# Performance work log

Measured on AMD Instinct MI355X. Metric: run time of the kernel, lower is better.

The kernel has to match this reference:

```python
import jax, jax.numpy as jnp
import numpy as np

B, N, D, H = 2, 2048, 1024, 16
DH = D // H
SCALE = DH ** -0.5

def setup_inputs() -> dict:
    key = jax.random.key(0)
    k1, k2, k3 = jax.random.split(key, 3)
    x = jax.random.normal(k1, (B, N, D), dtype=jnp.float32)
    W_qkv = jax.random.normal(k2, (3 * D, D), dtype=jnp.float32) * (D ** -0.5)
    W_out = jax.random.normal(k3, (D, D), dtype=jnp.float32) * (D ** -0.5)
    mask = jnp.tril(jnp.ones((N, N), dtype=jnp.int32))  # causal mask; 0 -> -inf
    return {"x": x, "mask": mask, "W_qkv": W_qkv, "W_out": W_out}

def reference(x, mask, W_qkv, W_out):
    b, n, d = x.shape
    qkv = x @ W_qkv.T                                   # [B,N,3D]
    qkv = qkv.reshape(b, n, 3, H, DH).transpose(2, 0, 3, 1, 4)  # [3,B,H,N,DH]
    q, k, v = qkv[0], qkv[1], qkv[2]
    attn = jnp.einsum('bhqd,bhkd->bhqk', q, k) * SCALE  # [B,H,N,N]
    attn = jnp.where(mask == 0, -jnp.inf, attn)
    attn = jax.nn.softmax(attn, axis=-1)
    out = jnp.einsum('bhqk,bhkd->bhqd', attn, v)        # [B,H,N,DH]
    out = out.transpose(0, 2, 1, 3).reshape(b, n, d)    # [B,N,D]
    return out @ W_out.T
```

## Files before the change

### kernel.cpp

```cpp
#include <hip/hip_runtime.h>
#include <hip/hip_bf16.h>


typedef __hip_bfloat16 bf16;
typedef short bf16x8 __attribute__((ext_vector_type(8)));
typedef short bf16x4 __attribute__((ext_vector_type(4)));
typedef float f32x4 __attribute__((ext_vector_type(4)));

#define QSCALE 0.1803368801111204f

typedef __attribute__((address_space(3))) unsigned int lds_u32;
typedef const __attribute__((address_space(1))) unsigned int glob_u32;

__device__ __forceinline__ void glds16(const void* g, void* l) {
    __builtin_amdgcn_global_load_lds((glob_u32*)g, (lds_u32*)l, 16, 0, 0);
}

__device__ __forceinline__ short f2bf(float f) {
    __hip_bfloat16 h = __float2bfloat16(f);
    return *reinterpret_cast<short*>(&h);
}

__device__ __forceinline__ unsigned pack_bf16(float a, float b) {
    unsigned au = __builtin_bit_cast(unsigned, a) + 0x8000u;
    unsigned bu = __builtin_bit_cast(unsigned, b) + 0x8000u;
    return __builtin_amdgcn_perm(bu, au, 0x07060302u);
}

__global__ void cast_all(const float* __restrict__ x, const float* __restrict__ wqkv,
                         const float* __restrict__ wout, bf16* __restrict__ xb,
                         bf16* __restrict__ wqb, bf16* __restrict__ wob) {
    int i = blockIdx.x * blockDim.x + threadIdx.x;
    const float* src; bf16* dst; int off;
    if (i < 1048576)      { src = x;    dst = xb;  off = i; }
    else if (i < 1835008) { src = wqkv; dst = wqb; off = i - 1048576; }
    else                  { src = wout; dst = wob; off = i - 1835008; }
    float4 f = reinterpret_cast<const float4*>(src)[off];
    short4 s;
    s.x = f2bf(f.x); s.y = f2bf(f.y); s.z = f2bf(f.z); s.w = f2bf(f.w);
    reinterpret_cast<short4*>(dst)[off] = s;
}

template<int EPI>
__global__ __launch_bounds__(256)
void gemm128(const bf16* __restrict__ A, const bf16* __restrict__ Bt,
             float* __restrict__ Cf,
             bf16* __restrict__ qp, bf16* __restrict__ kp, bf16* __restrict__ vp,
             int K, int Ncols) {
    __shared__ alignas(16) short As[2][4096];
    __shared__ alignas(16) short Bs[2][4096];

    const int tid = threadIdx.x;
    const int wave = tid >> 6, lane = tid & 63;
    const int quad = lane >> 4, l16 = lane & 15;
    const int wm = wave >> 1, wn = wave & 1;
    const int m0 = blockIdx.x * 128;
    const int n0 = blockIdx.y * 128;

    f32x4 acc[4][4] = {};

    const int srow = tid >> 2;
    const int skk  = (((tid & 3) ^ ((tid >> 3) & 3))) * 8;
    const bf16* Ag = A  + (size_t)(m0 + srow) * K + skk;
    const bf16* Bg = Bt + (size_t)(n0 + srow) * K + skk;
    const size_t rowskip = (size_t)64 * K;
    short* Asl = &As[0][0] + tid * 8;
    short* Bsl = &Bs[0][0] + tid * 8;

    const int xk = (quad ^ ((l16 >> 1) & 3)) * 8;
    const int arow = wm * 64 + l16;
    const int brow = wn * 64 + l16;

    const int KI = K >> 5;
    glds16(Ag, Asl);
    glds16(Ag + rowskip, Asl + 2048);
    glds16(Bg, Bsl);
    glds16(Bg + rowskip, Bsl + 2048);
    __syncthreads();

    int buf = 0;
    for (int ki = 0; ki < KI; ++ki) {
        if (ki + 1 < KI) {
            const bf16* ag = Ag + (ki + 1) * 32;
            const bf16* bg = Bg + (ki + 1) * 32;
            short* ad = Asl + (buf ^ 1) * 4096;
            short* bd = Bsl + (buf ^ 1) * 4096;
            glds16(ag, ad);
            glds16(ag + rowskip, ad + 2048);
            glds16(bg, bd);
            glds16(bg + rowskip, bd + 2048);
        }
        const short* ab = &As[buf][0];
        const short* bb = &Bs[buf][0];
        bf16x8 af[4], bf[4];
        #pragma unroll
        for (int mt = 0; mt < 4; ++mt)
            af[mt] = *reinterpret_cast<const bf16x8*>(ab + (arow + mt * 16) * 32 + xk);
        #pragma unroll
        for (int nt = 0; nt < 4; ++nt)
            bf[nt] = *reinterpret_cast<const bf16x8*>(bb + (brow + nt * 16) * 32 + xk);
        #pragma unroll
        for (int mt = 0; mt < 4; ++mt)
            #pragma unroll
            for (int nt = 0; nt < 4; ++nt)
                acc[mt][nt] = __builtin_amdgcn_mfma_f32_16x16x32_bf16(
                    af[mt], bf[nt], acc[mt][nt], 0, 0, 0);
        __syncthreads();
        buf ^= 1;
    }

    #pragma unroll
    for (int mt = 0; mt < 4; ++mt) {
        #pragma unroll
        for (int nt = 0; nt < 4; ++nt) {
            #pragma unroll
            for (int r = 0; r < 4; ++r) {
                int gm = m0 + wm * 64 + mt * 16 + quad * 4 + r;
                int gn = n0 + wn * 64 + nt * 16 + l16;
                float val = acc[mt][nt][r];
                if (EPI == 0) {
                    int sel = gn >> 10, rem = gn & 1023;
                    int h = rem >> 6, dh = rem & 63;
                    int b = gm >> 11, nq = gm & 2047;
                    if (sel == 0) val *= QSCALE;
                    bf16* dst = (sel == 0) ? qp : ((sel == 1) ? kp : vp);
                    dst[((((size_t)b * 16 + h) * 2048) + nq) * 64 + dh] = __float2bfloat16(val);
                } else {
                    Cf[(size_t)gm * Ncols + gn] = val;
                }
            }
        }
    }
}

__device__ __forceinline__ void attn_segment(
    const bf16* __restrict__ Qb, const bf16* __restrict__ Kb,
    const bf16* __restrict__ Vb, bf16* __restrict__ ao,
    float* __restrict__ Pslot, float* __restrict__ Lslot,
    short (*Ks)[64][72], short (*Vt)[64][68],
    int Q0, int jt0, int ntiles, bool withDiag, bool finalOut,
    int wave, int quad, int l16, int tid, int b, int h)
{
    const float NEG_INF = -__builtin_inff();
    const int qrowA = Q0 + wave * 16 + l16;
    const int qrowB = qrowA + 64;
    const bf16x8 qfA0 = *reinterpret_cast<const bf16x8*>(Qb + (size_t)qrowA * 64 + quad * 8);
    const bf16x8 qfA1 = *reinterpret_cast<const bf16x8*>(Qb + (size_t)qrowA * 64 + 32 + quad * 8);
    const bf16x8 qfB0 = *reinterpret_cast<const bf16x8*>(Qb + (size_t)qrowB * 64 + quad * 8);
    const bf16x8 qfB1 = *reinterpret_cast<const bf16x8*>(Qb + (size_t)qrowB * 64 + 32 + quad * 8);

    float lA = 0.f, lB = 0.f;
    f32x4 oA[4] = {}, oB[4] = {};

    const int krow = tid >> 2, kcol = (tid & 3) * 16;
    const int kb = (tid & 15) * 4, db = (tid >> 4) * 4;

    __syncthreads();
    {
        const bf16* K0 = Kb + (size_t)jt0 * 4096;
        const bf16* V0 = Vb + (size_t)jt0 * 4096;
        bf16x8 a0 = *reinterpret_cast<const bf16x8*>(K0 + (size_t)krow * 64 + kcol);
        bf16x8 a1 = *reinterpret_cast<const bf16x8*>(K0 + (size_t)krow * 64 + kcol + 8);
        bf16x4 L0 = *reinterpret_cast<const bf16x4*>(V0 + (size_t)(kb + 0) * 64 + db);
        bf16x4 L1 = *reinterpret_cast<const bf16x4*>(V0 + (size_t)(kb + 1) * 64 + db);
        bf16x4 L2 = *reinterpret_cast<const bf16x4*>(V0 + (size_t)(kb + 2) * 64 + db);
        bf16x4 L3 = *reinterpret_cast<const bf16x4*>(V0 + (size_t)(kb + 3) * 64 + db);
        *reinterpret_cast<bf16x8*>(&Ks[0][krow][kcol]) = a0;
        *reinterpret_cast<bf16x8*>(&Ks[0][krow][kcol + 8]) = a1;
        #pragma unroll
        for (int j = 0; j < 4; ++j) {
            bf16x4 w; w[0] = L0[j]; w[1] = L1[j]; w[2] = L2[j]; w[3] = L3[j];
            *reinterpret_cast<bf16x4*>(&Vt[0][db + j][kb]) = w;
        }
    }
    __syncthreads();

    int buf = 0;
    for (int i = 0; i < ntiles; ++i) {
        const bool diagA = withDiag && (i == ntiles - 2);
        const bool diagB = withDiag && (i == ntiles - 1);
        const bool pre = (i + 1 < ntiles);

        bf16x8 nk0, nk1; bf16x4 N0, N1, N2, N3;
        if (pre) {
            const bf16* Kn = Kb + (size_t)(jt0 + i + 1) * 4096;
            const bf16* Vn = Vb + (size_t)(jt0 + i + 1) * 4096;
            nk0 = *reinterpret_cast<const bf16x8*>(Kn + (size_t)krow * 64 + kcol);
            nk1 = *reinterpret_cast<const bf16x8*>(Kn + (size_t)krow * 64 + kcol + 8);
            N0 = *reinterpret_cast<const bf16x4*>(Vn + (size_t)(kb + 0) * 64 + db);
            N1 = *reinterpret_cast<const bf16x4*>(Vn + (size_t)(kb + 1) * 64 + db);
            N2 = *reinterpret_cast<const bf16x4*>(Vn + (size_t)(kb + 2) * 64 + db);
            N3 = *reinterpret_cast<const bf16x4*>(Vn + (size_t)(kb + 3) * 64 + db);
        }

        bf16x4 pkA[4], pkB[4];
        if (!diagA && !diagB) {
            #pragma unroll
            for (int t = 0; t < 4; ++t) {
                bf16x8 k0 = *reinterpret_cast<const bf16x8*>(&Ks[buf][16 * t + l16][quad * 8]);
                bf16x8 k1 = *reinterpret_cast<const bf16x8*>(&Ks[buf][16 * t + l16][32 + quad * 8]);
                f32x4 sA = {}, sB = {};
                sA = __builtin_amdgcn_mfma_f32_16x16x32_bf16(k0, qfA0, sA, 0, 0, 0);
                sA = __builtin_amdgcn_mfma_f32_16x16x32_bf16(k1, qfA1, sA, 0, 0, 0);
                sB = __builtin_amdgcn_mfma_f32_16x16x32_bf16(k0, qfB0, sB, 0, 0, 0);
                sB = __builtin_amdgcn_mfma_f32_16x16x32_bf16(k1, qfB1, sB, 0, 0, 0);
                float a0 = __builtin_amdgcn_exp2f(sA[0]);
                float a1 = __builtin_amdgcn_exp2f(sA[1]);
                float a2 = __builtin_amdgcn_exp2f(sA[2]);
                float a3 = __builtin_amdgcn_exp2f(sA[3]);
                float b0 = __builtin_amdgcn_exp2f(sB[0]);
                float b1 = __builtin_amdgcn_exp2f(sB[1]);
                float b2 = __builtin_amdgcn_exp2f(sB[2]);
                float b3 = __builtin_amdgcn_exp2f(sB[3]);
                lA += (a0 + a1) + (a2 + a3);
                lB += (b0 + b1) + (b2 + b3);
                unsigned* pa = reinterpret_cast<unsigned*>(&pkA[t]);
                pa[0] = pack_bf16(a0, a1); pa[1] = pack_bf16(a2, a3);
                unsigned* pb = reinterpret_cast<unsigned*>(&pkB[t]);
                pb[0] = pack_bf16(b0, b1); pb[1] = pack_bf16(b2, b3);
            }
            #pragma unroll
            for (int t = 0; t < 4; ++t)
                #pragma unroll
                for (int dt = 0; dt < 4; ++dt) {
                    bf16x4 vf = *reinterpret_cast<const bf16x4*>(
                        &Vt[buf][dt * 16 + l16][t * 16 + quad * 4]);
                    oA[dt] = __builtin_amdgcn_mfma_f32_16x16x16bf16_1k(vf, pkA[t], oA[dt], 0, 0, 0);
                    oB[dt] = __builtin_amdgcn_mfma_f32_16x16x16bf16_1k(vf, pkB[t], oB[dt], 0, 0, 0);
                }
        } else if (diagA) {
            #pragma unroll
            for (int t = 0; t < 4; ++t) {
                bf16x8 k0 = *reinterpret_cast<const bf16x8*>(&Ks[buf][16 * t + l16][quad * 8]);
                bf16x8 k1 = *reinterpret_cast<const bf16x8*>(&Ks[buf][16 * t + l16][32 + quad * 8]);
                f32x4 sB = {};
                sB = __builtin_amdgcn_mfma_f32_16x16x32_bf16(k0, qfB0, sB, 0, 0, 0);
                sB = __builtin_amdgcn_mfma_f32_16x16x32_bf16(k1, qfB1, sB, 0, 0, 0);
                float b0 = __builtin_amdgcn_exp2f(sB[0]);
                float b1 = __builtin_amdgcn_exp2f(sB[1]);
                float b2 = __builtin_amdgcn_exp2f(sB[2]);
                float b3 = __builtin_amdgcn_exp2f(sB[3]);
                lB += (b0 + b1) + (b2 + b3);
                unsigned* pb = reinterpret_cast<unsigned*>(&pkB[t]);
                pb[0] = pack_bf16(b0, b1); pb[1] = pack_bf16(b2, b3);
                if (t <= wave) {
                    f32x4 sA = {};
                    sA = __builtin_amdgcn_mfma_f32_16x16x32_bf16(k0, qfA0, sA, 0, 0, 0);
                    sA = __builtin_amdgcn_mfma_f32_16x16x32_bf16(k1, qfA1, sA, 0, 0, 0);
                    if (t == wave) {
                        #pragma unroll
                        for (int r = 0; r < 4; ++r)
                            if (quad * 4 + r > l16) sA[r] = NEG_INF;
                    }
                    float a0 = __builtin_amdgcn_exp2f(sA[0]);
                    float a1 = __builtin_amdgcn_exp2f(sA[1]);
                    float a2 = __builtin_amdgcn_exp2f(sA[2]);
                    float a3 = __builtin_amdgcn_exp2f(sA[3]);
                    lA += (a0 + a1) + (a2 + a3);
                    unsigned* pa = reinterpret_cast<unsigned*>(&pkA[t]);
                    pa[0] = pack_bf16(a0, a1); pa[1] = pack_bf16(a2, a3);
                }
            }
            #pragma unroll
            for (int t = 0; t < 4; ++t)
                #pragma unroll
                for (int dt = 0; dt < 4; ++dt) {
                    bf16x4 vf = *reinterpret_cast<const bf16x4*>(
                        &Vt[buf][dt * 16 + l16][t * 16 + quad * 4]);
                    oB[dt] = __builtin_amdgcn_mfma_f32_16x16x16bf16_1k(vf, pkB[t], oB[dt], 0, 0, 0);
                    if (t <= wave)
                        oA[dt] = __builtin_amdgcn_mfma_f32_16x16x16bf16_1k(vf, pkA[t], oA[dt], 0, 0, 0);
                }
        } else {
            #pragma unroll
            for (int t = 0; t < 4; ++t) {
                if (t <= wave) {
                    bf16x8 k0 = *reinterpret_cast<const bf16x8*>(&Ks[buf][16 * t + l16][quad * 8]);
                    bf16x8 k1 = *reinterpret_cast<const bf16x8*>(&Ks[buf][16 * t + l16][32 + quad * 8]);
                    f32x4 sB = {};
                    sB = __builtin_amdgcn_mfma_f32_16x16x32_bf16(k0, qfB0, sB, 0, 0, 0);
                    sB = __builtin_amdgcn_mfma_f32_16x16x32_bf16(k1, qfB1, sB, 0, 0, 0);
                    if (t == wave) {
                        #pragma unroll
                        for (int r = 0; r < 4; ++r)
                            if (quad * 4 + r > l16) sB[r] = NEG_INF;
                    }
                    float b0 = __builtin_amdgcn_exp2f(sB[0]);
                    float b1 = __builtin_amdgcn_exp2f(sB[1]);
                    float b2 = __builtin_amdgcn_exp2f(sB[2]);
                    float b3 = __builtin_amdgcn_exp2f(sB[3]);
                    lB += (b0 + b1) + (b2 + b3);
                    unsigned* pb = reinterpret_cast<unsigned*>(&pkB[t]);
                    pb[0] = pack_bf16(b0, b1); pb[1] = pack_bf16(b2, b3);
                }
            }
            #pragma unroll
            for (int t = 0; t < 4; ++t) {
                if (t <= wave) {
                    #pragma unroll
                    for (int dt = 0; dt < 4; ++dt) {
                        bf16x4 vf = *reinterpret_cast<const bf16x4*>(
                            &Vt[buf][dt * 16 + l16][t * 16 + quad * 4]);
                        oB[dt] = __builtin_amdgcn_mfma_f32_16x16x16bf16_1k(vf, pkB[t], oB[dt], 0, 0, 0);
                    }
                }
            }
        }

        if (pre) {
            *reinterpret_cast<bf16x8*>(&Ks[buf ^ 1][krow][kcol]) = nk0;
            *reinterpret_cast<bf16x8*>(&Ks[buf ^ 1][krow][kcol + 8]) = nk1;
            #pragma unroll
            for (int j = 0; j < 4; ++j) {
                bf16x4 w; w[0] = N0[j]; w[1] = N1[j]; w[2] = N2[j]; w[3] = N3[j];
                *reinterpret_cast<bf16x4*>(&Vt[buf ^ 1][db + j][kb]) = w;
            }
            __syncthreads();
            buf ^= 1;
        }
    }

    if (finalOut) {
        lA += __shfl_xor(lA, 16, 64);
        lA += __shfl_xor(lA, 32, 64);
        lB += __shfl_xor(lB, 16, 64);
        lB += __shfl_xor(lB, 32, 64);
        const float invA = 1.f / lA;
        const float invB = 1.f / lB;
        bf16* orowA = ao + ((size_t)b * 2048 + qrowA) * 1024 + h * 64;
        bf16* orowB = ao + ((size_t)b * 2048 + qrowB) * 1024 + h * 64;
        #pragma unroll
        for (int dt = 0; dt < 4; ++dt) {
            bf16x4 wA, wB;
            unsigned* ua = reinterpret_cast<unsigned*>(&wA);
            ua[0] = pack_bf16(oA[dt][0] * invA, oA[dt][1] * invA);
            ua[1] = pack_bf16(oA[dt][2] * invA, oA[dt][3] * invA);
            *reinterpret_cast<bf16x4*>(orowA + dt * 16 + quad * 4) = wA;
            unsigned* ub = reinterpret_cast<unsigned*>(&wB);
            ub[0] = pack_bf16(oB[dt][0] * invB, oB[dt][1] * invB);
            ub[1] = pack_bf16(oB[dt][2] * invB, oB[dt][3] * invB);
            *reinterpret_cast<bf16x4*>(orowB + dt * 16 + quad * 4) = wB;
        }
    } else {
        const int rrA = wave * 16 + l16;
        float* pA = Pslot + rrA * 64;
        float* pB = Pslot + (rrA + 64) * 64;
        #pragma unroll
        for (int dt = 0; dt < 4; ++dt) {
            *reinterpret_cast<f32x4*>(pA + dt * 16 + quad * 4) = oA[dt];
            *reinterpret_cast<f32x4*>(pB + dt * 16 + quad * 4) = oB[dt];
        }
        lA += __shfl_xor(lA, 16, 64);
        lA += __shfl_xor(lA, 32, 64);
        lB += __shfl_xor(lB, 16, 64);
        lB += __shfl_xor(lB, 32, 64);
        if (quad == 0) {
            Lslot[rrA] = lA;
            Lslot[rrA + 64] = lB;
        }
    }
}

__global__ __launch_bounds__(256)
void flash_split(const bf16* __restrict__ Q, const bf16* __restrict__ K,
                 const bf16* __restrict__ V, float* __restrict__ Ppart,
                 float* __restrict__ Lpart, bf16* __restrict__ ao) {
    __shared__ alignas(16) short Ks[2][64][72];
    __shared__ alignas(16) short Vt[2][64][68];

    const int tid = threadIdx.x;
    const int wave = tid >> 6, lane = tid & 63;
    const int quad = lane >> 4, l16 = lane & 15;
    const int bh = blockIdx.x;
    const int ys = blockIdx.y;
    const int p = ys & 7;
    const int qhi = 15 - p;
    const int b = bh >> 4, h = bh & 15;

    const bf16* Qb = Q + (size_t)bh * 2048 * 64;
    const bf16* Kb = K + (size_t)bh * 2048 * 64;
    const bf16* Vb = V + (size_t)bh * 2048 * 64;

    if (ys < 8) {
        attn_segment(Qb, Kb, Vb, ao, nullptr, nullptr, Ks, Vt,
                     p * 128, 0, 2 * p + 2, true, true,
                     wave, quad, l16, tid, b, h);
        float* Ps = Ppart + (size_t)(bh * 8 + p) * 8192;
        float* Ls = Lpart + (size_t)(bh * 8 + p) * 128;
        attn_segment(Qb, Kb, Vb, ao, Ps, Ls, Ks, Vt,
                     qhi * 128, 0, 15 - 2 * p, false, false,
                     wave, quad, l16, tid, b, h);
    } else {
        float* Ps = Ppart + (size_t)(256 + bh * 8 + p) * 8192;
        float* Ls = Lpart + (size_t)(256 + bh * 8 + p) * 128;
        attn_segment(Qb, Kb, Vb, ao, Ps, Ls, Ks, Vt,
                     qhi * 128, 15 - 2 * p, 17, true, false,
                     wave, quad, l16, tid, b, h);
    }
}

__global__ __launch_bounds__(256)
void combine(const float* __restrict__ Ppart, const float* __restrict__ Lpart,
             bf16* __restrict__ ao) {
    const int s = blockIdx.x;
    const int bh = s >> 3, p = s & 7;
    const int Q0 = (15 - p) * 128;
    const int b = bh >> 4, h = bh & 15;
    const int rr = threadIdx.x >> 1;
    const int dh0 = (threadIdx.x & 1) * 32;

    const float* p0 = Ppart + (size_t)s * 8192 + rr * 64 + dh0;
    const float* p1 = Ppart + (size_t)(256 + s) * 8192 + rr * 64 + dh0;
    const float inv = 1.f / (Lpart[(size_t)s * 128 + rr] +
                             Lpart[(size_t)(256 + s) * 128 + rr]);
    bf16* dst = ao + ((size_t)b * 2048 + Q0 + rr) * 1024 + h * 64 + dh0;
    #pragma unroll
    for (int j = 0; j < 32; j += 8) {
        f32x4 a0 = *reinterpret_cast<const f32x4*>(p0 + j);
        f32x4 a1 = *reinterpret_cast<const f32x4*>(p0 + j + 4);
        f32x4 c0 = *reinterpret_cast<const f32x4*>(p1 + j);
        f32x4 c1 = *reinterpret_cast<const f32x4*>(p1 + j + 4);
        bf16x8 w;
        unsigned* u = reinterpret_cast<unsigned*>(&w);
        u[0] = pack_bf16((a0[0] + c0[0]) * inv, (a0[1] + c0[1]) * inv);
        u[1] = pack_bf16((a0[2] + c0[2]) * inv, (a0[3] + c0[3]) * inv);
        u[2] = pack_bf16((a1[0] + c1[0]) * inv, (a1[1] + c1[1]) * inv);
        u[3] = pack_bf16((a1[2] + c1[2]) * inv, (a1[3] + c1[3]) * inv);
        *reinterpret_cast<bf16x8*>(dst + j) = w;
    }
}

extern "C" void kernel_launch(void* const* d_in, const int* in_sizes, int n_in,
                              void* d_out, int out_size, void* d_ws, size_t ws_size,
                              hipStream_t stream) {
    const float* x    = (const float*)d_in[0];
    const float* Wqkv = (const float*)d_in[2];
    const float* Wout = (const float*)d_in[3];
    float* out = (float*)d_out;

    char* ws = (char*)d_ws;
    bf16*  x_bf    = (bf16*)(ws);
    bf16*  wqkv_bf = (bf16*)(ws + (8ull << 20));
    float* Ppart   = (float*)(ws);
    bf16*  q       = (bf16*)(ws + (16ull << 20));
    bf16*  k       = (bf16*)(ws + (24ull << 20));
    bf16*  v       = (bf16*)(ws + (32ull << 20));
    bf16*  ao      = (bf16*)(ws + (40ull << 20));
    bf16*  wout_bf = (bf16*)(ws + (48ull << 20));
    float* Lpart   = (float*)(ws + (50ull << 20));

    cast_all<<<8192, 256, 0, stream>>>(x, Wqkv, Wout, x_bf, wqkv_bf, wout_bf);
    gemm128<0><<<dim3(32, 24), 256, 0, stream>>>(x_bf, wqkv_bf, nullptr, q, k, v, 1024, 3072);
    flash_split<<<dim3(32, 16), 256, 0, stream>>>(q, k, v, Ppart, Lpart, ao);
    combine<<<256, 256, 0, stream>>>(Ppart, Lpart, ao);
    gemm128<1><<<dim3(32, 8), 256, 0, stream>>>(ao, wout_bf, out, nullptr, nullptr, nullptr, 1024, 1024);
}
```

Measured before the change: 186.5 us.

## Split causal attention work into four balanced KV chunks per pair

The flash kernel now launches twice as many blocks. Each paired query tile's 34 KV tiles are split into four roughly equal chunks, and partial outputs are stored in bf16 instead of fp32. The combine kernel sums up to four partials per tile and also handles the low tiles that were split. This aims to improve load balance and occupancy (launch bounds 256,4) and to cut partial-output traffic, at the cost of more combine work and bf16 rounding in the unnormalised partial sums.

```diff
diff --git a/kernel.cpp b/kernel.cpp
--- a/kernel.cpp
+++ b/kernel.cpp
@@ -133,158 +133,140 @@
     }
 }
 
-__device__ __forceinline__ void attn_segment(
-    const bf16* __restrict__ Qb, const bf16* __restrict__ Kb,
-    const bf16* __restrict__ Vb, bf16* __restrict__ ao,
-    float* __restrict__ Pslot, float* __restrict__ Lslot,
-    short (*Ks)[64][72], short (*Vt)[64][68],
-    int Q0, int jt0, int ntiles, bool withDiag, bool finalOut,
-    int wave, int quad, int l16, int tid, int b, int h)
-{
+__global__ __launch_bounds__(256, 4)
+void flash_split(const bf16* __restrict__ Q, const bf16* __restrict__ K,
+                 const bf16* __restrict__ V, bf16* __restrict__ Opart,
+                 float* __restrict__ Lpart, bf16* __restrict__ ao) {
+    __shared__ alignas(16) short Ks[2][64][72];
+    __shared__ alignas(16) short Vt[2][64][68];
+
+    const int tid = threadIdx.x;
+    const int wave = tid >> 6, lane = tid & 63;
+    const int quad = lane >> 4, l16 = lane & 15;
+    const int bh = blockIdx.x;
+    const int y = blockIdx.y;
+    const int p = y >> 2, c = y & 3;
+    const int TL = 2 * p + 2;
+    const int a  = (c == 0) ? 0 : (c == 1) ? 9 : (c == 2) ? 18 : 26;
+    const int bnd = a + ((c < 2) ? 9 : 8);
+    const int b = bh >> 4, h = bh & 15;
     const float NEG_INF = -__builtin_inff();
-    const int qrowA = Q0 + wave * 16 + l16;
-    const int qrowB = qrowA + 64;
-    const bf16x8 qfA0 = *reinterpret_cast<const bf16x8*>(Qb + (size_t)qrowA * 64 + quad * 8);
-    const bf16x8 qfA1 = *reinterpret_cast<const bf16x8*>(Qb + (size_t)qrowA * 64 + 32 + quad * 8);
-    const bf16x8 qfB0 = *reinterpret_cast<const bf16x8*>(Qb + (size_t)qrowB * 64 + quad * 8);
-    const bf16x8 qfB1 = *reinterpret_cast<const bf16x8*>(Qb + (size_t)qrowB * 64 + 32 + quad * 8);
-
-    float lA = 0.f, lB = 0.f;
-    f32x4 oA[4] = {}, oB[4] = {};
+
+    const bf16* Qb = Q + (size_t)bh * 2048 * 64;
+    const bf16* Kb = K + (size_t)bh * 2048 * 64;
+    const bf16* Vb = V + (size_t)bh * 2048 * 64;
+
+    const int le0 = (bnd < TL) ? bnd : TL;
+    const bool hasLo = (a < le0);
+    const int hs = ((a > TL) ? a : TL) - TL;
+    const int he = bnd - TL;
+    const bool hasHi = (he > hs);
+    const int nseg = (hasLo ? 1 : 0) + (hasHi ? 1 : 0);
 
     const int krow = tid >> 2, kcol = (tid & 3) * 16;
     const int kb = (tid & 15) * 4, db = (tid >> 4) * 4;
 
-    __syncthreads();
-    {
-        const bf16* K0 = Kb + (size_t)jt0 * 4096;
-        const bf16* V0 = Vb + (size_t)jt0 * 4096;
-        bf16x8 a0 = *reinterpret_cast<const bf16x8*>(K0 + (size_t)krow * 64 + kcol);
-        bf16x8 a1 = *reinterpret_cast<const bf16x8*>(K0 + (size_t)krow * 64 + kcol + 8);
-        bf16x4 L0 = *reinterpret_cast<const bf16x4*>(V0 + (size_t)(kb + 0) * 64 + db);
-        bf16x4 L1 = *reinterpret_cast<const bf16x4*>(V0 + (size_t)(kb + 1) * 64 + db);
-        bf16x4 L2 = *reinterpret_cast<const bf16x4*>(V0 + (size_t)(kb + 2) * 64 + db);
-        bf16x4 L3 = *reinterpret_cast<const bf16x4*>(V0 + (size_t)(kb + 3) * 64 + db);
-        *reinterpret_cast<bf16x8*>(&Ks[0][krow][kcol]) = a0;
-        *reinterpret_cast<bf16x8*>(&Ks[0][krow][kcol + 8]) = a1;
-        #pragma unroll
-        for (int j = 0; j < 4; ++j) {
-            bf16x4 w; w[0] = L0[j]; w[1] = L1[j]; w[2] = L2[j]; w[3] = L3[j];
-            *reinterpret_cast<bf16x4*>(&Vt[0][db + j][kb]) = w;
-        }
-    }
-    __syncthreads();
-
-    int buf = 0;
-    for (int i = 0; i < ntiles; ++i) {
-        const bool diagA = withDiag && (i == ntiles - 2);
-        const bool diagB = withDiag && (i == ntiles - 1);
-        const bool pre = (i + 1 < ntiles);
-
-        bf16x8 nk0, nk1; bf16x4 N0, N1, N2, N3;
-        if (pre) {
-            const bf16* Kn = Kb + (size_t)(jt0 + i + 1) * 4096;
-            const bf16* Vn = Vb + (size_t)(jt0 + i + 1) * 4096;
-            nk0 = *reinterpret_cast<const bf16x8*>(Kn + (size_t)krow * 64 + kcol);
-            nk1 = *reinterpret_cast<const bf16x8*>(Kn + (size_t)krow * 64 + kcol + 8);
-            N0 = *reinterpret_cast<const bf16x4*>(Vn + (size_t)(kb + 0) * 64 + db);
-            N1 = *reinterpret_cast<const bf16x4*>(Vn + (size_t)(kb + 1) * 64 + db);
-            N2 = *reinterpret_cast<const bf16x4*>(Vn + (size_t)(kb + 2) * 64 + db);
-            N3 = *reinterpret_cast<const bf16x4*>(Vn + (size_t)(kb + 3) * 64 + db);
-        }
-
-        bf16x4 pkA[4], pkB[4];
-        if (!diagA && !diagB) {
-            #pragma unroll
-            for (int t = 0; t < 4; ++t) {
-                bf16x8 k0 = *reinterpret_cast<const bf16x8*>(&Ks[buf][16 * t + l16][quad * 8]);
-                bf16x8 k1 = *reinterpret_cast<const bf16x8*>(&Ks[buf][16 * t + l16][32 + quad * 8]);
-                f32x4 sA = {}, sB = {};
-                sA = __builtin_amdgcn_mfma_f32_16x16x32_bf16(k0, qfA0, sA, 0, 0, 0);
-                sA = __builtin_amdgcn_mfma_f32_16x16x32_bf16(k1, qfA1, sA, 0, 0, 0);
-                sB = __builtin_amdgcn_mfma_f32_16x16x32_bf16(k0, qfB0, sB, 0, 0, 0);
-                sB = __builtin_amdgcn_mfma_f32_16x16x32_bf16(k1, qfB1, sB, 0, 0, 0);
-                float a0 = __builtin_amdgcn_exp2f(sA[0]);
-                float a1 = __builtin_amdgcn_exp2f(sA[1]);
-                float a2 = __builtin_amdgcn_exp2f(sA[2]);
-                float a3 = __builtin_amdgcn_exp2f(sA[3]);
-                float b0 = __builtin_amdgcn_exp2f(sB[0]);
-                float b1 = __builtin_amdgcn_exp2f(sB[1]);
-                float b2 = __builtin_amdgcn_exp2f(sB[2]);
-                float b3 = __builtin_amdgcn_exp2f(sB[3]);
-                lA += (a0 + a1) + (a2 + a3);
-                lB += (b0 + b1) + (b2 + b3);
-                unsigned* pa = reinterpret_cast<unsigned*>(&pkA[t]);
-                pa[0] = pack_bf16(a0, a1); pa[1] = pack_bf16(a2, a3);
-                unsigned* pb = reinterpret_cast<unsigned*>(&pkB[t]);
-                pb[0] = pack_bf16(b0, b1); pb[1] = pack_bf16(b2, b3);
-            }
-            #pragma unroll
-            for (int t = 0; t < 4; ++t)
-                #pragma unroll
-                for (int dt = 0; dt < 4; ++dt) {
-                    bf16x4 vf = *reinterpret_cast<const bf16x4*>(
-                        &Vt[buf][dt * 16 + l16][t * 16 + quad * 4]);
-                    oA[dt] = __builtin_amdgcn_mfma_f32_16x16x16bf16_1k(vf, pkA[t], oA[dt], 0, 0, 0);
-                    oB[dt] = __builtin_amdgcn_mfma_f32_16x16x16bf16_1k(vf, pkB[t], oB[dt], 0, 0, 0);
-                }
-        } else if (diagA) {
-            #pragma unroll
-            for (int t = 0; t < 4; ++t) {
-                bf16x8 k0 = *reinterpret_cast<const bf16x8*>(&Ks[buf][16 * t + l16][quad * 8]);
-                bf16x8 k1 = *reinterpret_cast<const bf16x8*>(&Ks[buf][16 * t + l16][32 + quad * 8]);
-                f32x4 sB = {};
-                sB = __builtin_amdgcn_mfma_f32_16x16x32_bf16(k0, qfB0, sB, 0, 0, 0);
-                sB = __builtin_amdgcn_mfma_f32_16x16x32_bf16(k1, qfB1, sB, 0, 0, 0);
-                float b0 = __builtin_amdgcn_exp2f(sB[0]);
-                float b1 = __builtin_amdgcn_exp2f(sB[1]);
-                float b2 = __builtin_amdgcn_exp2f(sB[2]);
-                float b3 = __builtin_amdgcn_exp2f(sB[3]);
-                lB += (b0 + b1) + (b2 + b3);
-                unsigned* pb = reinterpret_cast<unsigned*>(&pkB[t]);
-                pb[0] = pack_bf16(b0, b1); pb[1] = pack_bf16(b2, b3);
-                if (t <= wave) {
-                    f32x4 sA = {};
+    for (int sgi = 0; sgi < nseg; ++sgi) {
+        const bool isLo = hasLo && (sgi == 0);
+        const int Q0  = (isLo ? p : (15 - p)) * 128;
+        const int jt0 = isLo ? a : hs;
+        const int nt  = isLo ? (le0 - a) : (he - hs);
+        const int T   = isLo ? TL : (34 - TL);
+        const bool fin = isLo && (a == 0) && (le0 == TL);
+        const int slot = ((bh * 8 + p) * 2 + (isLo ? 0 : 1)) * 4 + c;
+
+        const int qrowA = Q0 + wave * 16 + l16;
+        const int qrowB = qrowA + 64;
+        const bf16x8 qfA0 = *reinterpret_cast<const bf16x8*>(Qb + (size_t)qrowA * 64 + quad * 8);
+        const bf16x8 qfA1 = *reinterpret_cast<const bf16x8*>(Qb + (size_t)qrowA * 64 + 32 + quad * 8);
+        const bf16x8 qfB0 = *reinterpret_cast<const bf16x8*>(Qb + (size_t)qrowB * 64 + quad * 8);
+        const bf16x8 qfB1 = *reinterpret_cast<const bf16x8*>(Qb + (size_t)qrowB * 64 + 32 + quad * 8);
+
+        float lA = 0.f, lB = 0.f;
+        f32x4 oA[4] = {}, oB[4] = {};
+
+        __syncthreads();
+        {
+            const bf16* K0 = Kb + (size_t)jt0 * 4096;
+            const bf16* V0 = Vb + (size_t)jt0 * 4096;
+            bf16x8 a0 = *reinterpret_cast<const bf16x8*>(K0 + (size_t)krow * 64 + kcol);
+            bf16x8 a1 = *reinterpret_cast<const bf16x8*>(K0 + (size_t)krow * 64 + kcol + 8);
+            bf16x4 L0 = *reinterpret_cast<const bf16x4*>(V0 + (size_t)(kb + 0) * 64 + db);
+            bf16x4 L1 = *reinterpret_cast<const bf16x4*>(V0 + (size_t)(kb + 1) * 64 + db);
+            bf16x4 L2 = *reinterpret_cast<const bf16x4*>(V0 + (size_t)(kb + 2) * 64 + db);
+            bf16x4 L3 = *reinterpret_cast<const bf16x4*>(V0 + (size_t)(kb + 3) * 64 + db);
+            *reinterpret_cast<bf16x8*>(&Ks[0][krow][kcol]) = a0;
+            *reinterpret_cast<bf16x8*>(&Ks[0][krow][kcol + 8]) = a1;
+            #pragma unroll
+            for (int j = 0; j < 4; ++j) {
+                bf16x4 w; w[0] = L0[j]; w[1] = L1[j]; w[2] = L2[j]; w[3] = L3[j];
+                *reinterpret_cast<bf16x4*>(&Vt[0][db + j][kb]) = w;
+            }
+        }
+        __syncthreads();
+
+        int buf = 0;
+        for (int i = 0; i < nt; ++i) {
+            const int jabs = jt0 + i;
+            const bool diagA = (jabs == T - 2);
+            const bool diagB = (jabs == T - 1);
+            const bool pre = (i + 1 < nt);
+
+            bf16x8 nk0, nk1; bf16x4 N0, N1, N2, N3;
+            if (pre) {
+                const bf16* Kn = Kb + (size_t)(jabs + 1) * 4096;
+                const bf16* Vn = Vb + (size_t)(jabs + 1) * 4096;
+                nk0 = *reinterpret_cast<const bf16x8*>(Kn + (size_t)krow * 64 + kcol);
+                nk1 = *reinterpret_cast<const bf16x8*>(Kn + (size_t)krow * 64 + kcol + 8);
+                N0 = *reinterpret_cast<const bf16x4*>(Vn + (size_t)(kb + 0) * 64 + db);
+                N1 = *reinterpret_cast<const bf16x4*>(Vn + (size_t)(kb + 1) * 64 + db);
+                N2 = *reinterpret_cast<const bf16x4*>(Vn + (size_t)(kb + 2) * 64 + db);
+                N3 = *reinterpret_cast<const bf16x4*>(Vn + (size_t)(kb + 3) * 64 + db);
+            }
+
+            bf16x4 pkA[4], pkB[4];
+            if (!diagA && !diagB) {
+                #pragma unroll
+                for (int t = 0; t < 4; ++t) {
+                    bf16x8 k0 = *reinterpret_cast<const bf16x8*>(&Ks[buf][16 * t + l16][quad * 8]);
+                    bf16x8 k1 = *reinterpret_cast<const bf16x8*>(&Ks[buf][16 * t + l16][32 + quad * 8]);
+                    f32x4 sA = {}, sB = {};
                     sA = __builtin_amdgcn_mfma_f32_16x16x32_bf16(k0, qfA0, sA, 0, 0, 0);
                     sA = __builtin_amdgcn_mfma_f32_16x16x32_bf16(k1, qfA1, sA, 0, 0, 0);
-                    if (t == wave) {
-                        #pragma unroll
-                        for (int r = 0; r < 4; ++r)
-                            if (quad * 4 + r > l16) sA[r] = NEG_INF;
-                    }
+                    sB = __builtin_amdgcn_mfma_f32_16x16x32_bf16(k0, qfB0, sB, 0, 0, 0);
+                    sB = __builtin_amdgcn_mfma_f32_16x16x32_bf16(k1, qfB1, sB, 0, 0, 0);
                     float a0 = __builtin_amdgcn_exp2f(sA[0]);
                     float a1 = __builtin_amdgcn_exp2f(sA[1]);
                     float a2 = __builtin_amdgcn_exp2f(sA[2]);
                     float a3 = __builtin_amdgcn_exp2f(sA[3]);
+                    float b0 = __builtin_amdgcn_exp2f(sB[0]);
+                    float b1 = __builtin_amdgcn_exp2f(sB[1]);
+                    float b2 = __builtin_amdgcn_exp2f(sB[2]);
+                    float b3 = __builtin_amdgcn_exp2f(sB[3]);
                     lA += (a0 + a1) + (a2 + a3);
+                    lB += (b0 + b1) + (b2 + b3);
                     unsigned* pa = reinterpret_cast<unsigned*>(&pkA[t]);
                     pa[0] = pack_bf16(a0, a1); pa[1] = pack_bf16(a2, a3);
-                }
-            }
-            #pragma unroll
-            for (int t = 0; t < 4; ++t)
-                #pragma unroll
-                for (int dt = 0; dt < 4; ++dt) {
-                    bf16x4 vf = *reinterpret_cast<const bf16x4*>(
-                        &Vt[buf][dt * 16 + l16][t * 16 + quad * 4]);
-                    oB[dt] = __builtin_amdgcn_mfma_f32_16x16x16bf16_1k(vf, pkB[t], oB[dt], 0, 0, 0);
-                    if (t <= wave)
+                    unsigned* pb = reinterpret_cast<unsigned*>(&pkB[t]);
+                    pb[0] = pack_bf16(b0, b1); pb[1] = pack_bf16(b2, b3);
+                }
+                #pragma unroll
+                for (int t = 0; t < 4; ++t)
+                    #pragma unroll
+                    for (int dt = 0; dt < 4; ++dt) {
+                        bf16x4 vf = *reinterpret_cast<const bf16x4*>(
+                            &Vt[buf][dt * 16 + l16][t * 16 + quad * 4]);
                         oA[dt] = __builtin_amdgcn_mfma_f32_16x16x16bf16_1k(vf, pkA[t], oA[dt], 0, 0, 0);
-                }
-        } else {
-            #pragma unroll
-            for (int t = 0; t < 4; ++t) {
-                if (t <= wave) {
+                        oB[dt] = __builtin_amdgcn_mfma_f32_16x16x16bf16_1k(vf, pkB[t], oB[dt], 0, 0, 0);
+                    }
+            } else if (diagA) {
+                #pragma unroll
+                for (int t = 0; t < 4; ++t) {
                     bf16x8 k0 = *reinterpret_cast<const bf16x8*>(&Ks[buf][16 * t + l16][quad * 8]);
                     bf16x8 k1 = *reinterpret_cast<const bf16x8*>(&Ks[buf][16 * t + l16][32 + quad * 8]);
                     f32x4 sB = {};
                     sB = __builtin_amdgcn_mfma_f32_16x16x32_bf16(k0, qfB0, sB, 0, 0, 0);
                     sB = __builtin_amdgcn_mfma_f32_16x16x32_bf16(k1, qfB1, sB, 0, 0, 0);
-                    if (t == wave) {
-                        #pragma unroll
-                        for (int r = 0; r < 4; ++r)
-                            if (quad * 4 + r > l16) sB[r] = NEG_INF;
-                    }
                     float b0 = __builtin_amdgcn_exp2f(sB[0]);
                     float b1 = __builtin_amdgcn_exp2f(sB[1]);
                     float b2 = __builtin_amdgcn_exp2f(sB[2]);
@@ -292,141 +274,165 @@
                     lB += (b0 + b1) + (b2 + b3);
                     unsigned* pb = reinterpret_cast<unsigned*>(&pkB[t]);
                     pb[0] = pack_bf16(b0, b1); pb[1] = pack_bf16(b2, b3);
-                }
-            }
-            #pragma unroll
-            for (int t = 0; t < 4; ++t) {
-                if (t <= wave) {
+                    if (t <= wave) {
+                        f32x4 sA = {};
+                        sA = __builtin_amdgcn_mfma_f32_16x16x32_bf16(k0, qfA0, sA, 0, 0, 0);
+                        sA = __builtin_amdgcn_mfma_f32_16x16x32_bf16(k1, qfA1, sA, 0, 0, 0);
+                        if (t == wave) {
+                            #pragma unroll
+                            for (int r = 0; r < 4; ++r)
+                                if (quad * 4 + r > l16) sA[r] = NEG_INF;
+                        }
+                        float a0 = __builtin_amdgcn_exp2f(sA[0]);
+                        float a1 = __builtin_amdgcn_exp2f(sA[1]);
+                        float a2 = __builtin_amdgcn_exp2f(sA[2]);
+                        float a3 = __builtin_amdgcn_exp2f(sA[3]);
+                        lA += (a0 + a1) + (a2 + a3);
+                        unsigned* pa = reinterpret_cast<unsigned*>(&pkA[t]);
+                        pa[0] = pack_bf16(a0, a1); pa[1] = pack_bf16(a2, a3);
+                    }
+                }
+                #pragma unroll
+                for (int t = 0; t < 4; ++t)
                     #pragma unroll
                     for (int dt = 0; dt < 4; ++dt) {
                         bf16x4 vf = *reinterpret_cast<const bf16x4*>(
                             &Vt[buf][dt * 16 + l16][t * 16 + quad * 4]);
                         oB[dt] = __builtin_amdgcn_mfma_f32_16x16x16bf16_1k(vf, pkB[t], oB[dt], 0, 0, 0);
+                        if (t <= wave)
+                            oA[dt] = __builtin_amdgcn_mfma_f32_16x16x16bf16_1k(vf, pkA[t], oA[dt], 0, 0, 0);
                     }
-                }
-            }
-        }
-
-        if (pre) {
-            *reinterpret_cast<bf16x8*>(&Ks[buf ^ 1][krow][kcol]) = nk0;
-            *reinterpret_cast<bf16x8*>(&Ks[buf ^ 1][krow][kcol + 8]) = nk1;
-            #pragma unroll
-            for (int j = 0; j < 4; ++j) {
-                bf16x4 w; w[0] = N0[j]; w[1] = N1[j]; w[2] = N2[j]; w[3] = N3[j];
-                *reinterpret_cast<bf16x4*>(&Vt[buf ^ 1][db + j][kb]) = w;
-            }
-            __syncthreads();
-            buf ^= 1;
-        }
-    }
-
-    if (finalOut) {
+            } else {
+                #pragma unroll
+                for (int t = 0; t < 4; ++t) {
+                    if (t <= wave) {
+                        bf16x8 k0 = *reinterpret_cast<const bf16x8*>(&Ks[buf][16 * t + l16][quad * 8]);
+                        bf16x8 k1 = *reinterpret_cast<const bf16x8*>(&Ks[buf][16 * t + l16][32 + quad * 8]);
+                        f32x4 sB = {};
+                        sB = __builtin_amdgcn_mfma_f32_16x16x32_bf16(k0, qfB0, sB, 0, 0, 0);
+                        sB = __builtin_amdgcn_mfma_f32_16x16x32_bf16(k1, qfB1, sB, 0, 0, 0);
+                        if (t == wave) {
+                            #pragma unroll
+                            for (int r = 0; r < 4; ++r)
+                                if (quad * 4 + r > l16) sB[r] = NEG_INF;
+                        }
+                        float b0 = __builtin_amdgcn_exp2f(sB[0]);
+                        float b1 = __builtin_amdgcn_exp2f(sB[1]);
+                        float b2 = __builtin_amdgcn_exp2f(sB[2]);
+                        float b3 = __builtin_amdgcn_exp2f(sB[3]);
+                        lB += (b0 + b1) + (b2 + b3);
+                        unsigned* pb = reinterpret_cast<unsigned*>(&pkB[t]);
+                        pb[0] = pack_bf16(b0, b1); pb[1] = pack_bf16(b2, b3);
+                    }
+                }
+                #pragma unroll
+                for (int t = 0; t < 4; ++t) {
+                    if (t <= wave) {
+                        #pragma unroll
+                        for (int dt = 0; dt < 4; ++dt) {
+                            bf16x4 vf = *reinterpret_cast<const bf16x4*>(
+                                &Vt[buf][dt * 16 + l16][t * 16 + quad * 4]);
+                            oB[dt] = __builtin_amdgcn_mfma_f32_16x16x16bf16_1k(vf, pkB[t], oB[dt], 0, 0, 0);
+                        }
+                    }
+                }
+            }
+
+            if (pre) {
+                *reinterpret_cast<bf16x8*>(&Ks[buf ^ 1][krow][kcol]) = nk0;
+                *reinterpret_cast<bf16x8*>(&Ks[buf ^ 1][krow][kcol + 8]) = nk1;
+                #pragma unroll
+                for (int j = 0; j < 4; ++j) {
+                    bf16x4 w; w[0] = N0[j]; w[1] = N1[j]; w[2] = N2[j]; w[3] = N3[j];
+                    *reinterpret_cast<bf16x4*>(&Vt[buf ^ 1][db + j][kb]) = w;
+                }
+                __syncthreads();
+                buf ^= 1;
+            }
+        }
+
         lA += __shfl_xor(lA, 16, 64);
         lA += __shfl_xor(lA, 32, 64);
         lB += __shfl_xor(lB, 16, 64);
         lB += __shfl_xor(lB, 32, 64);
-        const float invA = 1.f / lA;
-        const float invB = 1.f / lB;
-        bf16* orowA = ao + ((size_t)b * 2048 + qrowA) * 1024 + h * 64;
-        bf16* orowB = ao + ((size_t)b * 2048 + qrowB) * 1024 + h * 64;
-        #pragma unroll
-        for (int dt = 0; dt < 4; ++dt) {
-            bf16x4 wA, wB;
-            unsigned* ua = reinterpret_cast<unsigned*>(&wA);
-            ua[0] = pack_bf16(oA[dt][0] * invA, oA[dt][1] * invA);
-            ua[1] = pack_bf16(oA[dt][2] * invA, oA[dt][3] * invA);
-            *reinterpret_cast<bf16x4*>(orowA + dt * 16 + quad * 4) = wA;
-            unsigned* ub = reinterpret_cast<unsigned*>(&wB);
-            ub[0] = pack_bf16(oB[dt][0] * invB, oB[dt][1] * invB);
-            ub[1] = pack_bf16(oB[dt][2] * invB, oB[dt][3] * invB);
-            *reinterpret_cast<bf16x4*>(orowB + dt * 16 + quad * 4) = wB;
-        }
-    } else {
-        const int rrA = wave * 16 + l16;
-        float* pA = Pslot + rrA * 64;
-        float* pB = Pslot + (rrA + 64) * 64;
-        #pragma unroll
-        for (int dt = 0; dt < 4; ++dt) {
-            *reinterpret_cast<f32x4*>(pA + dt * 16 + quad * 4) = oA[dt];
-            *reinterpret_cast<f32x4*>(pB + dt * 16 + quad * 4) = oB[dt];
-        }
-        lA += __shfl_xor(lA, 16, 64);
-        lA += __shfl_xor(lA, 32, 64);
-        lB += __shfl_xor(lB, 16, 64);
-        lB += __shfl_xor(lB, 32, 64);
-        if (quad == 0) {
-            Lslot[rrA] = lA;
-            Lslot[rrA + 64] = lB;
+        const int rr = wave * 16 + l16;
+        if (fin) {
+            const float invA = 1.f / lA;
+            const float invB = 1.f / lB;
+            bf16* orowA = ao + ((size_t)b * 2048 + qrowA) * 1024 + h * 64;
+            bf16* orowB = ao + ((size_t)b * 2048 + qrowB) * 1024 + h * 64;
+            #pragma unroll
+            for (int dt = 0; dt < 4; ++dt) {
+                bf16x4 wA, wB;
+                unsigned* ua = reinterpret_cast<unsigned*>(&wA);
+                ua[0] = pack_bf16(oA[dt][0] * invA, oA[dt][1] * invA);
+                ua[1] = pack_bf16(oA[dt][2] * invA, oA[dt][3] * invA);
+                *reinterpret_cast<bf16x4*>(orowA + dt * 16 + quad * 4) = wA;
+                unsigned* ub = reinterpret_cast<unsigned*>(&wB);
+                ub[0] = pack_bf16(oB[dt][0] * invB, oB[dt][1] * invB);
+                ub[1] = pack_bf16(oB[dt][2] * invB, oB[dt][3] * invB);
+                *reinterpret_cast<bf16x4*>(orowB + dt * 16 + quad * 4) = wB;
+            }
+        } else {
+            bf16* Os = Opart + (size_t)slot * 8192;
+            #pragma unroll
+            for (int dt = 0; dt < 4; ++dt) {
+                bf16x4 wA, wB;
+                unsigned* ua = reinterpret_cast<unsigned*>(&wA);
+                ua[0] = pack_bf16(oA[dt][0], oA[dt][1]);
+                ua[1] = pack_bf16(oA[dt][2], oA[dt][3]);
+                *reinterpret_cast<bf16x4*>(Os + rr * 64 + dt * 16 + quad * 4) = wA;
+                unsigned* ub = reinterpret_cast<unsigned*>(&wB);
+                ub[0] = pack_bf16(oB[dt][0], oB[dt][1]);
+                ub[1] = pack_bf16(oB[dt][2], oB[dt][3]);
+                *reinterpret_cast<bf16x4*>(Os + (rr + 64) * 64 + dt * 16 + quad * 4) = wB;
+            }
+            if (quad == 0) {
+                Lpart[(size_t)slot * 128 + rr] = lA;
+                Lpart[(size_t)slot * 128 + rr + 64] = lB;
+            }
         }
     }
 }
 
 __global__ __launch_bounds__(256)
-void flash_split(const bf16* __restrict__ Q, const bf16* __restrict__ K,
-                 const bf16* __restrict__ V, float* __restrict__ Ppart,
-                 float* __restrict__ Lpart, bf16* __restrict__ ao) {
-    __shared__ alignas(16) short Ks[2][64][72];
-    __shared__ alignas(16) short Vt[2][64][68];
-
-    const int tid = threadIdx.x;
-    const int wave = tid >> 6, lane = tid & 63;
-    const int quad = lane >> 4, l16 = lane & 15;
-    const int bh = blockIdx.x;
-    const int ys = blockIdx.y;
-    const int p = ys & 7;
-    const int qhi = 15 - p;
+void combine(const bf16* __restrict__ Opart, const float* __restrict__ Lpart,
+             bf16* __restrict__ ao) {
+    const int bh = blockIdx.x, y = blockIdx.y;
+    int p, row, cs, cn;
+    if (y < 8) { p = y;     row = 1; cs = (p < 4) ? 0 : 1; cn = (p < 4) ? 4 : 3; }
+    else       { p = y - 4; row = 0; cs = 0;               cn = 2; }
+    const int qt = row ? (15 - p) : p;
+    const int Q0 = qt * 128;
     const int b = bh >> 4, h = bh & 15;
-
-    const bf16* Qb = Q + (size_t)bh * 2048 * 64;
-    const bf16* Kb = K + (size_t)bh * 2048 * 64;
-    const bf16* Vb = V + (size_t)bh * 2048 * 64;
-
-    if (ys < 8) {
-        attn_segment(Qb, Kb, Vb, ao, nullptr, nullptr, Ks, Vt,
-                     p * 128, 0, 2 * p + 2, true, true,
-                     wave, quad, l16, tid, b, h);
-        float* Ps = Ppart + (size_t)(bh * 8 + p) * 8192;
-        float* Ls = Lpart + (size_t)(bh * 8 + p) * 128;
-        attn_segment(Qb, Kb, Vb, ao, Ps, Ls, Ks, Vt,
-                     qhi * 128, 0, 15 - 2 * p, false, false,
-                     wave, quad, l16, tid, b, h);
-    } else {
-        float* Ps = Ppart + (size_t)(256 + bh * 8 + p) * 8192;
-        float* Ls = Lpart + (size_t)(256 + bh * 8 + p) * 128;
-        attn_segment(Qb, Kb, Vb, ao, Ps, Ls, Ks, Vt,
-                     qhi * 128, 15 - 2 * p, 17, true, false,
-                     wave, quad, l16, tid, b, h);
-    }
-}
-
-__global__ __launch_bounds__(256)
-void combine(const float* __restrict__ Ppart, const float* __restrict__ Lpart,
-             bf16* __restrict__ ao) {
-    const int s = blockIdx.x;
-    const int bh = s >> 3, p = s & 7;
-    const int Q0 = (15 - p) * 128;
-    const int b = bh >> 4, h = bh & 15;
-    const int rr = threadIdx.x >> 1;
-    const int dh0 = (threadIdx.x & 1) * 32;
-
-    const float* p0 = Ppart + (size_t)s * 8192 + rr * 64 + dh0;
-    const float* p1 = Ppart + (size_t)(256 + s) * 8192 + rr * 64 + dh0;
-    const float inv = 1.f / (Lpart[(size_t)s * 128 + rr] +
-                             Lpart[(size_t)(256 + s) * 128 + rr]);
-    bf16* dst = ao + ((size_t)b * 2048 + Q0 + rr) * 1024 + h * 64 + dh0;
+    const size_t s0 = ((size_t)(bh * 8 + p) * 2 + row) * 4 + cs;
+    const bf16* O0 = Opart + s0 * 8192;
+    const float* L0 = Lpart + s0 * 128;
+
     #pragma unroll
-    for (int j = 0; j < 32; j += 8) {
-        f32x4 a0 = *reinterpret_cast<const f32x4*>(p0 + j);
-        f32x4 a1 = *reinterpret_cast<const f32x4*>(p0 + j + 4);
-        f32x4 c0 = *reinterpret_cast<const f32x4*>(p1 + j);
-        f32x4 c1 = *reinterpret_cast<const f32x4*>(p1 + j + 4);
-        bf16x8 w;
-        unsigned* u = reinterpret_cast<unsigned*>(&w);
-        u[0] = pack_bf16((a0[0] + c0[0]) * inv, (a0[1] + c0[1]) * inv);
-        u[1] = pack_bf16((a0[2] + c0[2]) * inv, (a0[3] + c0[3]) * inv);
-        u[2] = pack_bf16((a1[0] + c1[0]) * inv, (a1[1] + c1[1]) * inv);
-        u[3] = pack_bf16((a1[2] + c1[2]) * inv, (a1[3] + c1[3]) * inv);
-        *reinterpret_cast<bf16x8*>(dst + j) = w;
+    for (int it = 0; it < 4; ++it) {
+        const int idx = it * 2048 + threadIdx.x * 8;
+        const int r = idx >> 6, dh = idx & 63;
+        float lsum = 0.f;
+        for (int cc = 0; cc < cn; ++cc) lsum += L0[cc * 128 + r];
+        const float inv = 1.f / lsum;
+        float acc[8] = {};
+        for (int cc = 0; cc < cn; ++cc) {
+            const unsigned* u = reinterpret_cast<const unsigned*>(O0 + cc * 8192 + idx);
+            #pragma unroll
+            for (int jv = 0; jv < 4; ++jv) {
+                unsigned w = u[jv];
+                acc[2 * jv]     += __builtin_bit_cast(float, w << 16);
+                acc[2 * jv + 1] += __builtin_bit_cast(float, w & 0xFFFF0000u);
+            }
+        }
+        bf16x8 out;
+        unsigned* ou = reinterpret_cast<unsigned*>(&out);
+        ou[0] = pack_bf16(acc[0] * inv, acc[1] * inv);
+        ou[1] = pack_bf16(acc[2] * inv, acc[3] * inv);
+        ou[2] = pack_bf16(acc[4] * inv, acc[5] * inv);
+        ou[3] = pack_bf16(acc[6] * inv, acc[7] * inv);
+        *reinterpret_cast<bf16x8*>(ao + ((size_t)b * 2048 + Q0 + r) * 1024 + h * 64 + dh) = out;
     }
 }
 
@@ -441,17 +447,17 @@
     char* ws = (char*)d_ws;
     bf16*  x_bf    = (bf16*)(ws);
     bf16*  wqkv_bf = (bf16*)(ws + (8ull << 20));
-    float* Ppart   = (float*)(ws);
+    bf16*  wout_bf = (bf16*)(ws + (14ull << 20));
     bf16*  q       = (bf16*)(ws + (16ull << 20));
     bf16*  k       = (bf16*)(ws + (24ull << 20));
     bf16*  v       = (bf16*)(ws + (32ull << 20));
     bf16*  ao      = (bf16*)(ws + (40ull << 20));
-    bf16*  wout_bf = (bf16*)(ws + (48ull << 20));
-    float* Lpart   = (float*)(ws + (50ull << 20));
+    bf16*  Opart   = (bf16*)(ws + (48ull << 20));
+    float* Lpart   = (float*)(ws + (80ull << 20));
 
     cast_all<<<8192, 256, 0, stream>>>(x, Wqkv, Wout, x_bf, wqkv_bf, wout_bf);
     gemm128<0><<<dim3(32, 24), 256, 0, stream>>>(x_bf, wqkv_bf, nullptr, q, k, v, 1024, 3072);
-    flash_split<<<dim3(32, 16), 256, 0, stream>>>(q, k, v, Ppart, Lpart, ao);
-    combine<<<256, 256, 0, stream>>>(Ppart, Lpart, ao);
+    flash_split<<<dim3(32, 32), 256, 0, stream>>>(q, k, v, Opart, Lpart, ao);
+    combine<<<dim3(32, 12), 256, 0, stream>>>(Opart, Lpart, ao);
     gemm128<1><<<dim3(32, 8), 256, 0, stream>>>(ao, wout_bf, out, nullptr, nullptr, nullptr, 1024, 1024);
 }
```

After: 328.1 us. +75.9%, slower.
